# Kernel optimization log

Measured on AMD Instinct MI355X. Metric: run time of the kernel, lower is better.

## Reference

```python
import jax, jax.numpy as jnp
import numpy as np

GAMMA = 0.9
TEMPERATURE = 0.07
BASE_TEMPERATURE = 0.07
U_SIZE = 15_000_000
BSZ, N_VIEWS, DIM = 2048, 2, 256


def setup_inputs() -> dict:
    key = jax.random.key(0)
    kf, = jax.random.split(key, 1)
    feats = jax.random.normal(kf, (BSZ, N_VIEWS, DIM), dtype=jnp.float32)
    # contrastive features are unit-normalized in practice
    feats = feats / jnp.linalg.norm(feats, axis=-1, keepdims=True)
    index = jnp.arange(BSZ, dtype=jnp.int64) if jax.config.jax_enable_x64 else jnp.arange(BSZ, dtype=jnp.int32)
    u = jnp.zeros((U_SIZE, 1), dtype=jnp.float32)
    return {"index": index, "features": feats, "u": u}


def reference(index, features, u):
    B, V, D = features.shape          # bsz, n_views, dim
    N = B * V
    eye_b = jnp.eye(B, dtype=jnp.float32)

    # torch.cat(torch.unbind(features, dim=1), dim=0) -> [V*B, D], views stacked
    contrast_feature = jnp.transpose(features, (1, 0, 2)).reshape(N, D)
    anchor_feature = contrast_feature  # contrast_mode == 'all'

    # [N, N] similarity logits
    anchor_dot_contrast = jnp.matmul(anchor_feature, contrast_feature.T) / TEMPERATURE
    logits_max = jax.lax.stop_gradient(jnp.max(anchor_dot_contrast, axis=1, keepdims=True))
    logits = anchor_dot_contrast - logits_max

    # positive mask: tiled identity with self-contrast removed
    mask = jnp.tile(eye_b, (V, V))
    logits_mask = 1.0 - jnp.eye(N, dtype=jnp.float32)  # scatter of zeros on the diagonal
    pos_mask = mask * logits_mask
    neg_mask = 1.0 - pos_mask

    # detached negative exp-logits (EMA statistics)
    neg_exp_logits = jax.lax.stop_gradient(jnp.exp(logits) * neg_mask)

    # indexed EMA buffer update: u[index] = (1-g)*u[index] + g*rowsum[:B]
    row_sum = jnp.sum(neg_exp_logits, axis=1, keepdims=True)[:B]   # [B, 1]
    u_new = (1.0 - GAMMA) * u[index] + GAMMA * row_sum             # [B, 1]
    # (buffer write: u = u.at[index].set(u_new); only u_new is read below)

    p_neg_pairs = neg_exp_logits / jnp.tile(u_new, (V, 1))         # [N, N], detached numer/denom
    log_prob = logits - jnp.sum(p_neg_pairs * logits * neg_mask, axis=1, keepdims=True)

    mean_log_prob_pos = jnp.sum(pos_mask * log_prob, axis=1) / jnp.sum(pos_mask, axis=1)
    loss = -(TEMPERATURE / BASE_TEMPERATURE) * mean_log_prob_pos
    return loss.reshape(V, B).mean()
```

## Files before the change

kernel.cpp:

```cpp
#include <hip/hip_runtime.h>


#define BSZ   2048
#define NROW  4096
#define DDIM  256
#define NB64  64
#define NT2   (NB64 * (NB64 + 1) / 2)
#define C1    (1.4426950408889634f / 0.07f)
#define LN2   0.6931471805599453f

typedef __attribute__((ext_vector_type(8))) __bf16 bf16x8;
typedef __attribute__((ext_vector_type(4))) float f32x4;

__device__ __forceinline__ short f2bs(float x) {
    __bf16 b = (__bf16)x;
    return __builtin_bit_cast(short, b);
}

__device__ __forceinline__ const float* crow_ptr(const float* feats, int i) {
    return feats + (((i & (BSZ - 1)) * 2 + (i >> 11)) << 8);
}

__global__ __launch_bounds__(256) void prep_kernel(const float* __restrict__ feats,
        float* __restrict__ Szero, short* __restrict__ CmF) {
    int gid = blockIdx.x * 256 + threadIdx.x;
    if (gid < 2 * NROW) Szero[gid] = 0.0f;

    int quad = gid & 3;
    int l15  = (gid >> 2) & 15;
    int rt   = (gid >> 6) & 3;
    int k    = (gid >> 8) & 7;
    int b    = gid >> 12;
    int srow = (b << 6) + (rt << 4) + l15;
    int kel  = (k << 5) + (quad << 3);
    const float4* fp = (const float4*)(crow_ptr(feats, srow) + kel);
    float4 v0 = fp[0], v1 = fp[1];
    short h[8] = { f2bs(v0.x), f2bs(v0.y), f2bs(v0.z), f2bs(v0.w),
                   f2bs(v1.x), f2bs(v1.y), f2bs(v1.z), f2bs(v1.w) };
    *(int4*)(CmF + gid * 8) = *(int4*)h;
}

__global__ __launch_bounds__(64, 3) void gemm_sym(const short* __restrict__ CmF,
        float* __restrict__ S1, float* __restrict__ S2,
        float* __restrict__ Praw, float* __restrict__ Draw) {
    int lane = threadIdx.x;
    int quad = lane >> 4;
    int l15  = lane & 15;

    int t = blockIdx.x;
    int p = (int)((sqrtf(8.0f * (float)t + 1.0f) - 1.0f) * 0.5f);
    while ((p + 1) * (p + 2) / 2 <= t) ++p;
    while (p * (p + 1) / 2 > t) --p;
    int q = t - p * (p + 1) / 2;
    int rowBase = q << 6;
    int colBase = p << 6;
    bool offdiag = (p != q);

    int laneOff = ((l15 << 2) + quad) * 8;
    int aO = q * 16384 + laneOff;
    int bO = p * 16384 + laneOff;

    f32x4 acc[4][4];
    #pragma unroll
    for (int a = 0; a < 4; ++a)
        #pragma unroll
        for (int c = 0; c < 4; ++c) acc[a][c] = (f32x4){0.f, 0.f, 0.f, 0.f};

    bf16x8 aF[2][4], bF[2][4];
    #pragma unroll
    for (int rt = 0; rt < 4; ++rt) {
        aF[0][rt] = *(const bf16x8*)(CmF + aO + rt * 512);
        bF[0][rt] = *(const bf16x8*)(CmF + bO + rt * 512);
    }

    #pragma unroll
    for (int k = 0; k < 8; ++k) {
        int cur = k & 1;
        int nxt = cur ^ 1;
        if (k < 7) {
            #pragma unroll
            for (int rt = 0; rt < 4; ++rt) {
                aF[nxt][rt] = *(const bf16x8*)(CmF + aO + ((k + 1) * 4 + rt) * 512);
                bF[nxt][rt] = *(const bf16x8*)(CmF + bO + ((k + 1) * 4 + rt) * 512);
            }
        }
        __builtin_amdgcn_s_setprio(1);
        #pragma unroll
        for (int rt = 0; rt < 4; ++rt)
            #pragma unroll
            for (int ct = 0; ct < 4; ++ct)
                acc[rt][ct] = __builtin_amdgcn_mfma_f32_16x16x32_bf16(
                    aF[cur][rt], bF[cur][ct], acc[rt][ct], 0, 0, 0);
        __builtin_amdgcn_s_setprio(0);
    }

    float S1r[4][4] = {}, S2r[4][4] = {};
    float S1c[4] = {}, S2c[4] = {};
    #pragma unroll
    for (int rt = 0; rt < 4; ++rt) {
        #pragma unroll
        for (int ct = 0; ct < 4; ++ct) {
            #pragma unroll
            for (int r = 0; r < 4; ++r) {
                float d  = acc[rt][ct][r];
                float t0 = d * C1;
                float f  = __builtin_exp2f(t0);
                S1r[rt][r] += f;
                S2r[rt][r] = __builtin_fmaf(f, t0, S2r[rt][r]);
                if (offdiag) {
                    S1c[ct] += f;
                    S2c[ct] = __builtin_fmaf(f, t0, S2c[ct]);
                }
            }
        }
    }

    if (p == (q ^ 32)) {
        if (quad == (l15 >> 2)) {
            int r = l15 & 3;
            #pragma unroll
            for (int rt = 0; rt < 4; ++rt) {
                float t0 = acc[rt][rt][r] * C1;
                Praw[rowBase + rt * 16 + l15] = t0;
                Praw[colBase + rt * 16 + l15] = t0;
            }
        }
    }
    if (!offdiag) {
        if (quad == (l15 >> 2)) {
            int r = l15 & 3;
            #pragma unroll
            for (int rt = 0; rt < 4; ++rt)
                Draw[rowBase + rt * 16 + l15] = acc[rt][rt][r] * C1;
        }
    }

    #pragma unroll
    for (int rt = 0; rt < 4; ++rt) {
        #pragma unroll
        for (int r = 0; r < 4; ++r) {
            float e = S1r[rt][r], w = S2r[rt][r];
            #pragma unroll
            for (int off = 1; off < 16; off <<= 1) {
                e += __shfl_xor(e, off, 64);
                w += __shfl_xor(w, off, 64);
            }
            if (l15 == 0) {
                int grow = rowBase + rt * 16 + (quad << 2) + r;
                atomicAdd(&S1[grow], e);
                atomicAdd(&S2[grow], w);
            }
        }
    }
    if (offdiag) {
        #pragma unroll
        for (int ct = 0; ct < 4; ++ct) {
            float e = S1c[ct], w = S2c[ct];
            e += __shfl_xor(e, 16, 64);  w += __shfl_xor(w, 16, 64);
            e += __shfl_xor(e, 32, 64);  w += __shfl_xor(w, 32, 64);
            if (quad == 0) {
                int gcol = colBase + ct * 16 + l15;
                atomicAdd(&S1[gcol], e);
                atomicAdd(&S2[gcol], w);
            }
        }
    }
}

__global__ __launch_bounds__(1024) void finalize_kernel(const int* __restrict__ index,
        const float* __restrict__ u, const float* __restrict__ S1,
        const float* __restrict__ S2, const float* __restrict__ Praw,
        const float* __restrict__ Draw, float* __restrict__ out) {
    __shared__ float unew[BSZ];
    __shared__ float partial[16];
    int tid = threadIdx.x;
    for (int b = tid; b < BSZ; b += 1024) {
        float m  = -Draw[b];
        float tp = Praw[b] + m;
        float E  = __builtin_exp2f(m) * S1[b];
        unew[b] = 0.1f * u[index[b]] + 0.9f * (E - __builtin_exp2f(tp));
    }
    __syncthreads();
    float local = 0.0f;
    for (int i = tid; i < NROW; i += 1024) {
        float m   = -Draw[i];
        float tp  = Praw[i] + m;
        float etp = __builtin_exp2f(tp);
        float W   = __builtin_exp2f(m) * __builtin_fmaf(m, S1[i], S2[i]);
        local += tp - (W - etp * tp) / unew[i & (BSZ - 1)];
    }
    #pragma unroll
    for (int off = 32; off; off >>= 1) local += __shfl_xor(local, off, 64);
    if ((tid & 63) == 0) partial[tid >> 6] = local;
    __syncthreads();
    if (tid == 0) {
        float s = 0.0f;
        #pragma unroll
        for (int w = 0; w < 16; ++w) s += partial[w];
        out[0] = -LN2 * s / (float)NROW;
    }
}

extern "C" void kernel_launch(void* const* d_in, const int* in_sizes, int n_in,
                              void* d_out, int out_size, void* d_ws, size_t ws_size,
                              hipStream_t stream) {
    const int*   index = (const int*)d_in[0];
    const float* feats = (const float*)d_in[1];
    const float* u     = (const float*)d_in[2];
    float* out = (float*)d_out;

    float* S1   = (float*)d_ws;
    float* S2   = S1 + NROW;
    float* Praw = S2 + NROW;
    float* Draw = Praw + NROW;
    short* CmF  = (short*)((char*)d_ws + 131072);

    prep_kernel<<<1024, 256, 0, stream>>>(feats, S1, CmF);
    gemm_sym<<<NT2, 64, 0, stream>>>(CmF, S1, S2, Praw, Draw);
    finalize_kernel<<<1, 1024, 0, stream>>>(index, u, S1, S2, Praw, Draw, out);
}
```

Measured before the change: 114.2 us.

## Split GEMM tiles in half and fuse finalize into GEMM via completion counters

```diff
diff --git a/kernel.cpp b/kernel.cpp
--- a/kernel.cpp
+++ b/kernel.cpp
@@ -3,9 +3,10 @@
 
 #define BSZ   2048
 #define NROW  4096
-#define DDIM  256
 #define NB64  64
 #define NT2   (NB64 * (NB64 + 1) / 2)
+#define NBLK  (NT2 * 2)
+#define PAIR_TGT 254
 #define C1    (1.4426950408889634f / 0.07f)
 #define LN2   0.6931471805599453f
 
@@ -21,11 +22,8 @@
     return feats + (((i & (BSZ - 1)) * 2 + (i >> 11)) << 8);
 }
 
-__global__ __launch_bounds__(256) void prep_kernel(const float* __restrict__ feats,
-        float* __restrict__ Szero, short* __restrict__ CmF) {
-    int gid = blockIdx.x * 256 + threadIdx.x;
-    if (gid < 2 * NROW) Szero[gid] = 0.0f;
-
+__device__ __forceinline__ void pack_unit(const float* __restrict__ feats,
+                                          short* __restrict__ CmF, int gid) {
     int quad = gid & 3;
     int l15  = (gid >> 2) & 15;
     int rt   = (gid >> 6) & 3;
@@ -40,14 +38,59 @@
     *(int4*)(CmF + gid * 8) = *(int4*)h;
 }
 
-__global__ __launch_bounds__(64, 3) void gemm_sym(const short* __restrict__ CmF,
+__global__ __launch_bounds__(256) void prep_kernel(const float* __restrict__ feats,
+        float* __restrict__ S1, short* __restrict__ CmF, float* __restrict__ out) {
+    int gid = blockIdx.x * 256 + threadIdx.x;
+    if (gid < 2 * NROW) S1[gid] = 0.0f;
+    else if (gid < 2 * NROW + 32) ((int*)(S1 + 4 * NROW))[gid - 2 * NROW] = 0;
+    else if (gid == 2 * NROW + 32) out[0] = 0.0f;
+    pack_unit(feats, CmF, gid);
+}
+
+__device__ __forceinline__ void finalize_pair(int b, int lane,
+        float* S1, float* S2, float* Praw, float* Draw,
+        const int* __restrict__ index, const float* __restrict__ u,
+        float* __restrict__ out) {
+    __threadfence();
+    int rlo = (b << 6) + lane;
+    int rhi = rlo + BSZ;
+    float S1lo = __hip_atomic_load(&S1[rlo], __ATOMIC_RELAXED, __HIP_MEMORY_SCOPE_AGENT);
+    float S2lo = __hip_atomic_load(&S2[rlo], __ATOMIC_RELAXED, __HIP_MEMORY_SCOPE_AGENT);
+    float Plo  = __hip_atomic_load(&Praw[rlo], __ATOMIC_RELAXED, __HIP_MEMORY_SCOPE_AGENT);
+    float Dlo  = __hip_atomic_load(&Draw[rlo], __ATOMIC_RELAXED, __HIP_MEMORY_SCOPE_AGENT);
+    float S1hi = __hip_atomic_load(&S1[rhi], __ATOMIC_RELAXED, __HIP_MEMORY_SCOPE_AGENT);
+    float S2hi = __hip_atomic_load(&S2[rhi], __ATOMIC_RELAXED, __HIP_MEMORY_SCOPE_AGENT);
+    float Phi  = __hip_atomic_load(&Praw[rhi], __ATOMIC_RELAXED, __HIP_MEMORY_SCOPE_AGENT);
+    float Dhi  = __hip_atomic_load(&Draw[rhi], __ATOMIC_RELAXED, __HIP_MEMORY_SCOPE_AGENT);
+
+    float mlo = -Dlo, mhi = -Dhi;
+    float tplo = Plo + mlo, tphi = Phi + mhi;
+    float Elo = __builtin_exp2f(mlo) * S1lo;
+    float unew = 0.1f * u[index[rlo]] + 0.9f * (Elo - __builtin_exp2f(tplo));
+
+    float Wlo = __builtin_exp2f(mlo) * __builtin_fmaf(mlo, S1lo, S2lo);
+    float Whi = __builtin_exp2f(mhi) * __builtin_fmaf(mhi, S1hi, S2hi);
+    float etplo = __builtin_exp2f(tplo);
+    float etphi = __builtin_exp2f(tphi);
+    float local = (tplo - (Wlo - etplo * tplo) / unew)
+                + (tphi - (Whi - etphi * tphi) / unew);
+    #pragma unroll
+    for (int off = 32; off; off >>= 1) local += __shfl_xor(local, off, 64);
+    if (lane == 0) atomicAdd(out, -LN2 * local / (float)NROW);
+}
+
+__global__ __launch_bounds__(64, 4) void gemm_sym(const short* __restrict__ CmF,
         float* __restrict__ S1, float* __restrict__ S2,
-        float* __restrict__ Praw, float* __restrict__ Draw) {
+        float* __restrict__ Praw, float* __restrict__ Draw,
+        int* __restrict__ cnt, const int* __restrict__ index,
+        const float* __restrict__ u, float* __restrict__ out) {
     int lane = threadIdx.x;
     int quad = lane >> 4;
     int l15  = lane & 15;
 
-    int t = blockIdx.x;
+    int bh = blockIdx.x;
+    int h  = bh & 1;
+    int t  = bh >> 1;
     int p = (int)((sqrtf(8.0f * (float)t + 1.0f) - 1.0f) * 0.5f);
     while ((p + 1) * (p + 2) / 2 <= t) ++p;
     while (p * (p + 1) / 2 > t) --p;
@@ -57,21 +100,20 @@
     bool offdiag = (p != q);
 
     int laneOff = ((l15 << 2) + quad) * 8;
-    int aO = q * 16384 + laneOff;
-    int bO = p * 16384 + laneOff;
-
-    f32x4 acc[4][4];
-    #pragma unroll
-    for (int a = 0; a < 4; ++a)
+    const short* aB = CmF + q * 16384 + laneOff + (h * 2) * 512;
+    const short* bB = CmF + p * 16384 + laneOff;
+
+    f32x4 acc[2][4];
+    #pragma unroll
+    for (int a = 0; a < 2; ++a)
         #pragma unroll
         for (int c = 0; c < 4; ++c) acc[a][c] = (f32x4){0.f, 0.f, 0.f, 0.f};
 
-    bf16x8 aF[2][4], bF[2][4];
-    #pragma unroll
-    for (int rt = 0; rt < 4; ++rt) {
-        aF[0][rt] = *(const bf16x8*)(CmF + aO + rt * 512);
-        bF[0][rt] = *(const bf16x8*)(CmF + bO + rt * 512);
-    }
+    bf16x8 aF[2][2], bF[2][4];
+    #pragma unroll
+    for (int j = 0; j < 2; ++j) aF[0][j] = *(const bf16x8*)(aB + j * 512);
+    #pragma unroll
+    for (int ct = 0; ct < 4; ++ct) bF[0][ct] = *(const bf16x8*)(bB + ct * 512);
 
     #pragma unroll
     for (int k = 0; k < 8; ++k) {
@@ -79,34 +121,35 @@
         int nxt = cur ^ 1;
         if (k < 7) {
             #pragma unroll
-            for (int rt = 0; rt < 4; ++rt) {
-                aF[nxt][rt] = *(const bf16x8*)(CmF + aO + ((k + 1) * 4 + rt) * 512);
-                bF[nxt][rt] = *(const bf16x8*)(CmF + bO + ((k + 1) * 4 + rt) * 512);
-            }
+            for (int j = 0; j < 2; ++j)
+                aF[nxt][j] = *(const bf16x8*)(aB + (k + 1) * 2048 + j * 512);
+            #pragma unroll
+            for (int ct = 0; ct < 4; ++ct)
+                bF[nxt][ct] = *(const bf16x8*)(bB + (k + 1) * 2048 + ct * 512);
         }
         __builtin_amdgcn_s_setprio(1);
         #pragma unroll
-        for (int rt = 0; rt < 4; ++rt)
+        for (int j = 0; j < 2; ++j)
             #pragma unroll
             for (int ct = 0; ct < 4; ++ct)
-                acc[rt][ct] = __builtin_amdgcn_mfma_f32_16x16x32_bf16(
-                    aF[cur][rt], bF[cur][ct], acc[rt][ct], 0, 0, 0);
+                acc[j][ct] = __builtin_amdgcn_mfma_f32_16x16x32_bf16(
+                    aF[cur][j], bF[cur][ct], acc[j][ct], 0, 0, 0);
         __builtin_amdgcn_s_setprio(0);
     }
 
-    float S1r[4][4] = {}, S2r[4][4] = {};
+    float S1r[2][4] = {}, S2r[2][4] = {};
     float S1c[4] = {}, S2c[4] = {};
     #pragma unroll
-    for (int rt = 0; rt < 4; ++rt) {
+    for (int j = 0; j < 2; ++j) {
         #pragma unroll
         for (int ct = 0; ct < 4; ++ct) {
             #pragma unroll
             for (int r = 0; r < 4; ++r) {
-                float d  = acc[rt][ct][r];
+                float d  = acc[j][ct][r];
                 float t0 = d * C1;
                 float f  = __builtin_exp2f(t0);
-                S1r[rt][r] += f;
-                S2r[rt][r] = __builtin_fmaf(f, t0, S2r[rt][r]);
+                S1r[j][r] += f;
+                S2r[j][r] = __builtin_fmaf(f, t0, S2r[j][r]);
                 if (offdiag) {
                     S1c[ct] += f;
                     S2c[ct] = __builtin_fmaf(f, t0, S2c[ct]);
@@ -115,38 +158,37 @@
         }
     }
 
-    if (p == (q ^ 32)) {
-        if (quad == (l15 >> 2)) {
-            int r = l15 & 3;
-            #pragma unroll
-            for (int rt = 0; rt < 4; ++rt) {
-                float t0 = acc[rt][rt][r] * C1;
-                Praw[rowBase + rt * 16 + l15] = t0;
-                Praw[colBase + rt * 16 + l15] = t0;
-            }
-        }
-    }
-    if (!offdiag) {
-        if (quad == (l15 >> 2)) {
-            int r = l15 & 3;
-            #pragma unroll
-            for (int rt = 0; rt < 4; ++rt)
-                Draw[rowBase + rt * 16 + l15] = acc[rt][rt][r] * C1;
-        }
-    }
-
-    #pragma unroll
-    for (int rt = 0; rt < 4; ++rt) {
+    if (p == (q ^ 32) && quad == (l15 >> 2)) {
+        int r = l15 & 3;
+        #pragma unroll
+        for (int j = 0; j < 2; ++j) {
+            int rt = 2 * h + j;
+            float t0 = acc[j][rt][r] * C1;
+            Praw[rowBase + rt * 16 + l15] = t0;
+            Praw[colBase + rt * 16 + l15] = t0;
+        }
+    }
+    if (!offdiag && quad == (l15 >> 2)) {
+        int r = l15 & 3;
+        #pragma unroll
+        for (int j = 0; j < 2; ++j) {
+            int rt = 2 * h + j;
+            Draw[rowBase + rt * 16 + l15] = acc[j][rt][r] * C1;
+        }
+    }
+
+    #pragma unroll
+    for (int j = 0; j < 2; ++j) {
         #pragma unroll
         for (int r = 0; r < 4; ++r) {
-            float e = S1r[rt][r], w = S2r[rt][r];
+            float e = S1r[j][r], w = S2r[j][r];
             #pragma unroll
             for (int off = 1; off < 16; off <<= 1) {
                 e += __shfl_xor(e, off, 64);
                 w += __shfl_xor(w, off, 64);
             }
             if (l15 == 0) {
-                int grow = rowBase + rt * 16 + (quad << 2) + r;
+                int grow = rowBase + (2 * h + j) * 16 + (quad << 2) + r;
                 atomicAdd(&S1[grow], e);
                 atomicAdd(&S2[grow], w);
             }
@@ -165,40 +207,24 @@
             }
         }
     }
-}
-
-__global__ __launch_bounds__(1024) void finalize_kernel(const int* __restrict__ index,
-        const float* __restrict__ u, const float* __restrict__ S1,
-        const float* __restrict__ S2, const float* __restrict__ Praw,
-        const float* __restrict__ Draw, float* __restrict__ out) {
-    __shared__ float unew[BSZ];
-    __shared__ float partial[16];
-    int tid = threadIdx.x;
-    for (int b = tid; b < BSZ; b += 1024) {
-        float m  = -Draw[b];
-        float tp = Praw[b] + m;
-        float E  = __builtin_exp2f(m) * S1[b];
-        unew[b] = 0.1f * u[index[b]] + 0.9f * (E - __builtin_exp2f(tp));
-    }
-    __syncthreads();
-    float local = 0.0f;
-    for (int i = tid; i < NROW; i += 1024) {
-        float m   = -Draw[i];
-        float tp  = Praw[i] + m;
-        float etp = __builtin_exp2f(tp);
-        float W   = __builtin_exp2f(m) * __builtin_fmaf(m, S1[i], S2[i]);
-        local += tp - (W - etp * tp) / unew[i & (BSZ - 1)];
-    }
-    #pragma unroll
-    for (int off = 32; off; off >>= 1) local += __shfl_xor(local, off, 64);
-    if ((tid & 63) == 0) partial[tid >> 6] = local;
-    __syncthreads();
-    if (tid == 0) {
-        float s = 0.0f;
-        #pragma unroll
-        for (int w = 0; w < 16; ++w) s += partial[w];
-        out[0] = -LN2 * s / (float)NROW;
-    }
+
+    __threadfence();
+    int fp0 = -1, fp1 = -1;
+    if (lane == 0) {
+        int prA = q & 31, prB = p & 31;
+        int o = __hip_atomic_fetch_add(&cnt[prA], 1, __ATOMIC_ACQ_REL,
+                                       __HIP_MEMORY_SCOPE_AGENT);
+        if (o == PAIR_TGT - 1) fp0 = prA;
+        if (prB != prA) {
+            o = __hip_atomic_fetch_add(&cnt[prB], 1, __ATOMIC_ACQ_REL,
+                                       __HIP_MEMORY_SCOPE_AGENT);
+            if (o == PAIR_TGT - 1) fp1 = prB;
+        }
+    }
+    fp0 = __shfl(fp0, 0, 64);
+    fp1 = __shfl(fp1, 0, 64);
+    if (fp0 >= 0) finalize_pair(fp0, lane, S1, S2, Praw, Draw, index, u, out);
+    if (fp1 >= 0) finalize_pair(fp1, lane, S1, S2, Praw, Draw, index, u, out);
 }
 
 extern "C" void kernel_launch(void* const* d_in, const int* in_sizes, int n_in,
@@ -213,9 +239,9 @@
     float* S2   = S1 + NROW;
     float* Praw = S2 + NROW;
     float* Draw = Praw + NROW;
+    int*   cnt  = (int*)(S1 + 4 * NROW);
     short* CmF  = (short*)((char*)d_ws + 131072);
 
-    prep_kernel<<<1024, 256, 0, stream>>>(feats, S1, CmF);
-    gemm_sym<<<NT2, 64, 0, stream>>>(CmF, S1, S2, Praw, Draw);
-    finalize_kernel<<<1, 1024, 0, stream>>>(index, u, S1, S2, Praw, Draw, out);
-}
+    prep_kernel<<<1024, 256, 0, stream>>>(feats, S1, CmF, out);
+    gemm_sym<<<NBLK, 64, 0, stream>>>(CmF, S1, S2, Praw, Draw, cnt, index, u, out);
+}
```

Result: slower. 428.0 us (+274.9%).
